# Optimization experiments

Measured on AMD Instinct MI355X. Metric: run time of the kernel, lower is better.

## Reference

```python
import jax, jax.numpy as jnp
import numpy as np

B, T, F, H, L = 256, 512, 64, 256, 2
DH = 2 * H          # decoder hidden size (bidirectional encoder concat)
OUT, OSL = 2, 20    # output_size, output_seq_len


def gru_cell(x, h, Wih, Whh, bih, bhh):
    # PyTorch GRU cell, gate order (r, z, n)
    gi = x @ Wih.T + bih
    gh = h @ Whh.T + bhh
    ir, iz, inn = jnp.split(gi, 3, axis=-1)
    hr, hz, hn = jnp.split(gh, 3, axis=-1)
    r = jax.nn.sigmoid(ir + hr)
    z = jax.nn.sigmoid(iz + hz)
    n = jnp.tanh(inn + r * hn)
    return (1.0 - z) * n + z * h


def setup_inputs() -> dict:
    key = jax.random.key(0)
    ks = iter(jax.random.split(key, 32))
    def p(shape, scale=0.05):
        return jax.random.normal(next(ks), shape, dtype=jnp.float32) * scale
    inp = {
        "x": p((B, T, F), 1.0),
        "start_token": jnp.zeros((1, 1, OUT), jnp.float32),
        # encoder layer 0 (input F), layer 1 (input 2H); axis 0 = direction (fwd, bwd)
        "enc_Wih0": p((2, 3 * H, F)), "enc_Whh0": p((2, 3 * H, H)),
        "enc_bih0": p((2, 3 * H)),   "enc_bhh0": p((2, 3 * H)),
        "enc_Wih1": p((2, 3 * H, 2 * H)), "enc_Whh1": p((2, 3 * H, H)),
        "enc_bih1": p((2, 3 * H)),   "enc_bhh1": p((2, 3 * H)),
        # decoder: unidirectional, hidden DH; layer0 input OUT, layer1 input DH
        "dec_Wih0": p((3 * DH, OUT)), "dec_Whh0": p((3 * DH, DH)),
        "dec_bih0": p((3 * DH,)),    "dec_bhh0": p((3 * DH,)),
        "dec_Wih1": p((3 * DH, DH)), "dec_Whh1": p((3 * DH, DH)),
        "dec_bih1": p((3 * DH,)),    "dec_bhh1": p((3 * DH,)),
        "fc_W": p((OUT, DH)), "fc_b": p((OUT,)),
    }
    return inp


def _run_dir(xs, Wih, Whh, bih, bhh, reverse):
    # xs: [T, B, Fin] -> (ys [T, B, H], h_T [B, H])
    h0 = jnp.zeros((xs.shape[1], Whh.shape[1]), xs.dtype)
    def step(h, xt):
        hn = gru_cell(xt, h, Wih, Whh, bih, bhh)
        return hn, hn
    hT, ys = jax.lax.scan(step, h0, xs, reverse=reverse)
    return ys, hT


def reference(x, start_token,
              enc_Wih0, enc_Whh0, enc_bih0, enc_bhh0,
              enc_Wih1, enc_Whh1, enc_bih1, enc_bhh1,
              dec_Wih0, dec_Whh0, dec_bih0, dec_bhh0,
              dec_Wih1, dec_Whh1, dec_bih1, dec_bhh1,
              fc_W, fc_b):
    b = x.shape[0]
    xs = jnp.swapaxes(x, 0, 1)  # [T, B, F]
    enc_layers = [(enc_Wih0, enc_Whh0, enc_bih0, enc_bhh0),
                  (enc_Wih1, enc_Whh1, enc_bih1, enc_bhh1)]
    hiddens = []
    layer_in = xs
    for (Wih, Whh, bih, bhh) in enc_layers:
        yf, hf = _run_dir(layer_in, Wih[0], Whh[0], bih[0], bhh[0], reverse=False)
        yb, hb = _run_dir(layer_in, Wih[1], Whh[1], bih[1], bhh[1], reverse=True)
        layer_in = jnp.concatenate([yf, yb], axis=-1)   # [T, B, 2H]
        hiddens.append(jnp.concatenate([hf, hb], axis=-1))  # [B, 2H] = cat(fwd, bwd)
    inp0 = jnp.broadcast_to(start_token, (b, 1, OUT))[:, 0]  # [B, OUT]
    def dec_step(carry, _):
        inp, (h0, h1) = carry
        h0n = gru_cell(inp, h0, dec_Wih0, dec_Whh0, dec_bih0, dec_bhh0)
        h1n = gru_cell(h0n, h1, dec_Wih1, dec_Whh1, dec_bih1, dec_bhh1)
        pred = h1n @ fc_W.T + fc_b
        return (pred, (h0n, h1n)), pred
    _, preds = jax.lax.scan(dec_step, (inp0, (hiddens[0], hiddens[1])), None, length=OSL)
    return jnp.swapaxes(preds, 0, 1)  # [B, OSL, OUT]
```

## Files before the change

### kernel.cpp

```cpp
#include <hip/hip_runtime.h>
#include <hip/hip_bf16.h>
#include <stdint.h>
#include <stddef.h>


typedef __bf16 bf16_t;
typedef bf16_t bf16x8 __attribute__((ext_vector_type(8)));
typedef float  f32x4  __attribute__((ext_vector_type(4)));

#define B_   256
#define T_   512
#define F_   64
#define H_   256
#define G_   768
#define DH_  512
#define DG_  1536
#define OSL_ 20

__device__ __forceinline__ float sigm(float x) {
    float e = __builtin_amdgcn_exp2f(-1.442695040888963f * x);
    return __builtin_amdgcn_rcpf(1.0f + e);
}
__device__ __forceinline__ float tanh_(float x) {
    float e = __builtin_amdgcn_exp2f(-2.885390081777927f * x);
    return __builtin_amdgcn_rcpf(1.0f + e) * 2.0f - 1.0f;
}

__device__ __forceinline__ bf16x8 load_f32x8_as_bf16(const float* p) {
    f32x4 u = *(const f32x4*)p;
    f32x4 v = *(const f32x4*)(p + 4);
    bf16x8 r;
    r[0]=(bf16_t)u[0]; r[1]=(bf16_t)u[1]; r[2]=(bf16_t)u[2]; r[3]=(bf16_t)u[3];
    r[4]=(bf16_t)v[0]; r[5]=(bf16_t)v[1]; r[6]=(bf16_t)v[2]; r[7]=(bf16_t)v[3];
    return r;
}


__global__ void cast_f32_bf16(const float* __restrict__ src, bf16_t* __restrict__ dst, int n) {
    int i = blockIdx.x * 256 + threadIdx.x;
    if (i < n) dst[i] = (bf16_t)src[i];
}

__global__ void weff_prep(const float* __restrict__ wih0d, const float* __restrict__ fcw,
                          const float* __restrict__ fcb, const float* __restrict__ bih0d,
                          const float* __restrict__ st, bf16_t* __restrict__ weff,
                          float* __restrict__ beff, float* __restrict__ ov) {
    int tid = blockIdx.x * 256 + threadIdx.x;
    if (tid >= DG_ * DH_) return;
    int g = tid >> 9, k = tid & 511;
    float a0 = wih0d[g * 2], a1 = wih0d[g * 2 + 1];
    weff[tid] = (bf16_t)(a0 * fcw[k] + a1 * fcw[DH_ + k]);
    if (k == 0) {
        beff[g] = a0 * fcb[0] + a1 * fcb[1] + bih0d[g];
        ov[g]   = a0 * st[0]  + a1 * st[1]  + bih0d[g];
    }
}

__global__ __launch_bounds__(256) void gemm_gi(
    const float* __restrict__ x, const bf16_t* __restrict__ xcat,
    const bf16_t* __restrict__ Bt, bf16_t* __restrict__ gi, int t0, int K) {
    __shared__ bf16_t As[128 * 64];
    __shared__ bf16_t Bs[128 * 64];
    int m0 = blockIdx.x * 128, n0 = blockIdx.y * 128;
    int tid = threadIdx.x;
    int lane = tid & 63, w = tid >> 6;
    int col = lane & 15, quad = lane >> 4;
    int qm = (w >> 1) * 64, qn = (w & 1) * 64;

    int tl = m0 >> 8;
    int bbase = m0 & 255;
    int t_real = t0 + tl;
    if (n0 >= 768) t_real = (T_ - 1) - t_real;

    f32x4 acc[4][4] = {};
    for (int k0 = 0; k0 < K; k0 += 64) {
        __syncthreads();
#pragma unroll
        for (int i = 0; i < 4; i++) {
            int c = i * 256 + tid;
            int m = c >> 3, kc = c & 7;
            int kcs = kc ^ (m & 7);
            bf16x8 av;
            if (K == 64) {
                av = load_f32x8_as_bf16(x + ((size_t)(bbase + m) * T_ + t_real) * F_ + kcs * 8);
            } else {
                av = *(const bf16x8*)(xcat + ((size_t)t_real * B_ + bbase + m) * DH_ + k0 + kcs * 8);
            }
            *(bf16x8*)(&As[c * 8]) = av;
            *(bf16x8*)(&Bs[c * 8]) = *(const bf16x8*)(Bt + (size_t)(n0 + m) * K + k0 + kcs * 8);
        }
        __syncthreads();
#pragma unroll
        for (int kt = 0; kt < 2; kt++) {
            bf16x8 a[4], b[4];
#pragma unroll
            for (int mt = 0; mt < 4; mt++) {
                int r = qm + mt * 16 + col;
                a[mt] = *(const bf16x8*)(&As[(r * 8 + ((kt * 4 + quad) ^ (r & 7))) * 8]);
                int rn = qn + mt * 16 + col;
                b[mt] = *(const bf16x8*)(&Bs[(rn * 8 + ((kt * 4 + quad) ^ (rn & 7))) * 8]);
            }
#pragma unroll
            for (int mt = 0; mt < 4; mt++)
#pragma unroll
                for (int nt = 0; nt < 4; nt++)
                    acc[mt][nt] = __builtin_amdgcn_mfma_f32_16x16x32_bf16(a[mt], b[nt], acc[mt][nt], 0, 0, 0);
        }
    }
#pragma unroll
    for (int mt = 0; mt < 4; mt++)
#pragma unroll
        for (int nt = 0; nt < 4; nt++)
#pragma unroll
            for (int i = 0; i < 4; i++) {
                int row = m0 + qm + mt * 16 + quad * 4 + i;
                int cg  = n0 + qn + nt * 16 + col;
                gi[(size_t)row * DG_ + cg] = (bf16_t)acc[mt][nt][i];
            }
}

__global__ __launch_bounds__(512) void gru_scan(
    const bf16_t* __restrict__ gi, int t0, int tc,
    const bf16_t* __restrict__ whh,
    const float* __restrict__ bih, const float* __restrict__ bhh,
    float* __restrict__ hstate, bf16_t* __restrict__ y, float* __restrict__ hT) {
    __shared__ bf16_t gi_lds[16 * 768];
    __shared__ bf16_t h_lds[2 * 16 * 264];

    int dir = blockIdx.x >> 4;
    int b0  = (blockIdx.x & 15) * 16;
    int tid = threadIdx.x;
    int w = tid >> 6, lane = tid & 63, col = lane & 15, quad = lane >> 4;

    bf16x8 wf[3][2][8];
    const bf16_t* wbase = whh + (size_t)dir * G_ * H_;
#pragma unroll
    for (int g = 0; g < 3; g++)
#pragma unroll
        for (int nt = 0; nt < 2; nt++) {
            int row = g * 256 + w * 32 + nt * 16 + col;
#pragma unroll
            for (int kt = 0; kt < 8; kt++)
                wf[g][nt][kt] = *(const bf16x8*)(wbase + (size_t)row * H_ + kt * 32 + quad * 8);
        }
    float brz[2][2], bin_[2], bhn[2];
#pragma unroll
    for (int nt = 0; nt < 2; nt++) {
        int j = w * 32 + nt * 16 + col;
        brz[0][nt] = bih[dir * G_ + j] + bhh[dir * G_ + j];
        brz[1][nt] = bih[dir * G_ + 256 + j] + bhh[dir * G_ + 256 + j];
        bin_[nt]   = bih[dir * G_ + 512 + j];
        bhn[nt]    = bhh[dir * G_ + 512 + j];
    }
    int bb[3], oo[3];
#pragma unroll
    for (int it = 0; it < 3; it++) {
        int c = it * 512 + tid;
        bb[it] = c / 96;
        oo[it] = (c % 96) * 8;
    }
    float hold[2][4];
#pragma unroll
    for (int nt = 0; nt < 2; nt++)
#pragma unroll
        for (int i = 0; i < 4; i++) {
            int j = w * 32 + nt * 16 + col;
            hold[nt][i] = t0 ? hstate[dir * 65536 + (b0 + quad * 4 + i) * 256 + j] : 0.0f;
        }
    for (int i = tid; i < 16 * 264; i += 512) {
        int b = i / 264, j = i % 264;
        float v = (t0 && j < 256) ? hstate[dir * 65536 + (b0 + b) * 256 + j] : 0.0f;
        h_lds[i] = (bf16_t)v;
    }
#pragma unroll
    for (int it = 0; it < 3; it++) {
        int c = it * 512 + tid;
        *(bf16x8*)(&gi_lds[c * 8]) =
            *(const bf16x8*)(gi + ((size_t)0 * B_ + b0 + bb[it]) * DG_ + dir * G_ + oo[it]);
    }
    __syncthreads();

    for (int s = 0; s < tc; s++) {
        int par = s & 1;
        int t = t0 + s;
        int sn = (s + 1 < tc) ? (s + 1) : s;

        bf16x8 pg[3];
#pragma unroll
        for (int it = 0; it < 3; it++)
            pg[it] = *(const bf16x8*)(gi + ((size_t)sn * B_ + b0 + bb[it]) * DG_ + dir * G_ + oo[it]);

        f32x4 acc[3][2] = {};
        const bf16_t* hcur = &h_lds[par * 4224];
#pragma unroll
        for (int kt = 0; kt < 8; kt++) {
            bf16x8 af = *(const bf16x8*)(hcur + col * 264 + kt * 32 + quad * 8);
#pragma unroll
            for (int g = 0; g < 3; g++)
#pragma unroll
                for (int nt = 0; nt < 2; nt++)
                    acc[g][nt] = __builtin_amdgcn_mfma_f32_16x16x32_bf16(af, wf[g][nt][kt], acc[g][nt], 0, 0, 0);
        }

        bf16_t* hnext = &h_lds[(par ^ 1) * 4224];
        int tp = dir ? (T_ - 1 - t) : t;
#pragma unroll
        for (int nt = 0; nt < 2; nt++) {
            int j = w * 32 + nt * 16 + col;
#pragma unroll
            for (int i = 0; i < 4; i++) {
                int b = quad * 4 + i;
                float gr = acc[0][nt][i] + (float)gi_lds[b * 768 + j]       + brz[0][nt];
                float gz = acc[1][nt][i] + (float)gi_lds[b * 768 + 256 + j] + brz[1][nt];
                float gn = (float)gi_lds[b * 768 + 512 + j] + bin_[nt];
                float r = sigm(gr), z = sigm(gz);
                float n = tanh_(gn + r * (acc[2][nt][i] + bhn[nt]));
                float hv = (1.0f - z) * n + z * hold[nt][i];
                hold[nt][i] = hv;
                hnext[b * 264 + j] = (bf16_t)hv;
                if (y) y[((size_t)tp * B_ + b0 + b) * DH_ + dir * H_ + j] = (bf16_t)hv;
                if (t == T_ - 1) hT[(size_t)(b0 + b) * DH_ + dir * H_ + j] = hv;
            }
        }
        __syncthreads();
#pragma unroll
        for (int it = 0; it < 3; it++)
            *(bf16x8*)(&gi_lds[(it * 512 + tid) * 8]) = pg[it];
        __syncthreads();
    }
#pragma unroll
    for (int nt = 0; nt < 2; nt++)
#pragma unroll
        for (int i = 0; i < 4; i++) {
            int j = w * 32 + nt * 16 + col;
            hstate[dir * 65536 + (b0 + quad * 4 + i) * 256 + j] = hold[nt][i];
        }
}

__global__ __launch_bounds__(256) void dec_cell(
    const float* __restrict__ xsrc, const bf16_t* __restrict__ Wx,
    const float* __restrict__ bx, const float* __restrict__ ov,
    const float* __restrict__ hin, const bf16_t* __restrict__ Wh,
    const float* __restrict__ bh, float* __restrict__ hout,
    float* __restrict__ hist) {
    int jblk = blockIdx.x & 7;
    int b0   = (blockIdx.x >> 3) * 16;
    int tid = threadIdx.x, w = tid >> 6, lane = tid & 63, col = lane & 15, quad = lane >> 4;
    int j = jblk * 64 + w * 16 + col;
    bool do_gi = (ov == nullptr);

    f32x4 agi[3] = {}, agh[3] = {};
#pragma unroll 4
    for (int kt = 0; kt < 16; kt++) {
        bf16x8 ah = load_f32x8_as_bf16(hin + (size_t)(b0 + col) * DH_ + kt * 32 + quad * 8);
#pragma unroll
        for (int g = 0; g < 3; g++) {
            bf16x8 bw = *(const bf16x8*)(Wh + (size_t)(g * DH_ + j) * DH_ + kt * 32 + quad * 8);
            agh[g] = __builtin_amdgcn_mfma_f32_16x16x32_bf16(ah, bw, agh[g], 0, 0, 0);
        }
        if (do_gi) {
            bf16x8 ax = load_f32x8_as_bf16(xsrc + (size_t)(b0 + col) * DH_ + kt * 32 + quad * 8);
#pragma unroll
            for (int g = 0; g < 3; g++) {
                bf16x8 bw = *(const bf16x8*)(Wx + (size_t)(g * DH_ + j) * DH_ + kt * 32 + quad * 8);
                agi[g] = __builtin_amdgcn_mfma_f32_16x16x32_bf16(ax, bw, agi[g], 0, 0, 0);
            }
        }
    }
#pragma unroll
    for (int i = 0; i < 4; i++) {
        int b = b0 + quad * 4 + i;
        float gr, gz, gn;
        if (do_gi) {
            gr = agi[0][i] + bx[j];
            gz = agi[1][i] + bx[DH_ + j];
            gn = agi[2][i] + bx[2 * DH_ + j];
        } else {
            gr = ov[j]; gz = ov[DH_ + j]; gn = ov[2 * DH_ + j];
        }
        float hr = agh[0][i] + bh[j];
        float hz = agh[1][i] + bh[DH_ + j];
        float hn = agh[2][i] + bh[2 * DH_ + j];
        float r = sigm(gr + hr), z = sigm(gz + hz);
        float n = tanh_(gn + r * hn);
        float hold = hin[(size_t)b * DH_ + j];
        float hv = (1.0f - z) * n + z * hold;
        hout[(size_t)b * DH_ + j] = hv;
        if (hist) hist[(size_t)b * DH_ + j] = hv;
    }
}

__global__ __launch_bounds__(256) void fc_all(
    const float* __restrict__ hist, const float* __restrict__ fcw,
    const float* __restrict__ fcb, float* __restrict__ out) {
    int t  = blockIdx.x >> 4;
    int b0 = (blockIdx.x & 15) * 16;
    int tid = threadIdx.x;
    int bl = tid >> 4, o = (tid >> 3) & 1, part = tid & 7;
    const float* hp = hist + ((size_t)t * B_ + b0 + bl) * DH_;
    const float* wp = fcw + o * DH_;
    float s = 0.0f;
    for (int k = part * 64; k < part * 64 + 64; k += 4) {
        f32x4 hv = *(const f32x4*)(hp + k);
        f32x4 wv = *(const f32x4*)(wp + k);
        s += hv[0] * wv[0] + hv[1] * wv[1] + hv[2] * wv[2] + hv[3] * wv[3];
    }
    s += __shfl_down(s, 4); s += __shfl_down(s, 2); s += __shfl_down(s, 1);
    if (part == 0) out[(size_t)(b0 + bl) * (OSL_ * 2) + t * 2 + o] = s + fcb[o];
}


#define OFF_WIH0E 0ull
#define OFF_WHH0E 196608ull
#define OFF_WIH1E 983040ull
#define OFF_WHH1E 2555904ull
#define OFF_WDHH0 3342336ull
#define OFF_WDIH1 4915200ull
#define OFF_WDHH1 6488064ull
#define OFF_WEFF  8060928ull
#define OFF_BEFF  9633792ull
#define OFF_OV    9658368ull
#define OFF_H0A   9682944ull
#define OFF_H0B   10207232ull
#define OFF_H1A   10731520ull
#define OFF_H1B   11255808ull
#define OFF_HST   11780096ull
#define OFF_HIST  12304384ull
#define OFF_XCAT  22790144ull
#define OFF_GI    157007872ull

extern "C" void kernel_launch(void* const* d_in, const int* in_sizes, int n_in,
                              void* d_out, int out_size, void* d_ws, size_t ws_size,
                              hipStream_t stream) {
    const float* x      = (const float*)d_in[0];
    const float* st     = (const float*)d_in[1];
    const float* eWih0  = (const float*)d_in[2];
    const float* eWhh0  = (const float*)d_in[3];
    const float* ebih0  = (const float*)d_in[4];
    const float* ebhh0  = (const float*)d_in[5];
    const float* eWih1  = (const float*)d_in[6];
    const float* eWhh1  = (const float*)d_in[7];
    const float* ebih1  = (const float*)d_in[8];
    const float* ebhh1  = (const float*)d_in[9];
    const float* dWih0  = (const float*)d_in[10];
    const float* dWhh0  = (const float*)d_in[11];
    const float* dbih0  = (const float*)d_in[12];
    const float* dbhh0  = (const float*)d_in[13];
    const float* dWih1  = (const float*)d_in[14];
    const float* dWhh1  = (const float*)d_in[15];
    const float* dbih1  = (const float*)d_in[16];
    const float* dbhh1  = (const float*)d_in[17];
    const float* fcW    = (const float*)d_in[18];
    const float* fcb    = (const float*)d_in[19];

    char* ws = (char*)d_ws;
    bf16_t* wih0e = (bf16_t*)(ws + OFF_WIH0E);
    bf16_t* whh0e = (bf16_t*)(ws + OFF_WHH0E);
    bf16_t* wih1e = (bf16_t*)(ws + OFF_WIH1E);
    bf16_t* whh1e = (bf16_t*)(ws + OFF_WHH1E);
    bf16_t* wdhh0 = (bf16_t*)(ws + OFF_WDHH0);
    bf16_t* wdih1 = (bf16_t*)(ws + OFF_WDIH1);
    bf16_t* wdhh1 = (bf16_t*)(ws + OFF_WDHH1);
    bf16_t* weff  = (bf16_t*)(ws + OFF_WEFF);
    float*  beff  = (float*)(ws + OFF_BEFF);
    float*  ovp   = (float*)(ws + OFF_OV);
    float*  h0buf[2] = { (float*)(ws + OFF_H0A), (float*)(ws + OFF_H0B) };
    float*  h1buf[2] = { (float*)(ws + OFF_H1A), (float*)(ws + OFF_H1B) };
    float*  hstate = (float*)(ws + OFF_HST);
    float*  hist  = (float*)(ws + OFF_HIST);
    bf16_t* xcat  = (bf16_t*)(ws + OFF_XCAT);
    bf16_t* gi    = (bf16_t*)(ws + OFF_GI);

    int Tc = 512;
    while (Tc > 8 && OFF_GI + (unsigned long long)Tc * 786432ull > (unsigned long long)ws_size)
        Tc >>= 1;
    int nch = T_ / Tc;

    cast_f32_bf16<<<(2*G_*F_ + 255)/256, 256, 0, stream>>>(eWih0, wih0e, 2*G_*F_);
    cast_f32_bf16<<<(2*G_*H_ + 255)/256, 256, 0, stream>>>(eWhh0, whh0e, 2*G_*H_);
    cast_f32_bf16<<<(2*G_*DH_ + 255)/256, 256, 0, stream>>>(eWih1, wih1e, 2*G_*DH_);
    cast_f32_bf16<<<(2*G_*H_ + 255)/256, 256, 0, stream>>>(eWhh1, whh1e, 2*G_*H_);
    cast_f32_bf16<<<(DG_*DH_ + 255)/256, 256, 0, stream>>>(dWhh0, wdhh0, DG_*DH_);
    cast_f32_bf16<<<(DG_*DH_ + 255)/256, 256, 0, stream>>>(dWih1, wdih1, DG_*DH_);
    cast_f32_bf16<<<(DG_*DH_ + 255)/256, 256, 0, stream>>>(dWhh1, wdhh1, DG_*DH_);
    weff_prep<<<(DG_*DH_ + 255)/256, 256, 0, stream>>>(dWih0, fcW, fcb, dbih0, st, weff, beff, ovp);

    for (int c = 0; c < nch; c++) {
        gemm_gi<<<dim3(Tc * 2, 12), 256, 0, stream>>>(x, nullptr, wih0e, gi, c * Tc, 64);
        gru_scan<<<32, 512, 0, stream>>>(gi, c * Tc, Tc, whh0e, ebih0, ebhh0, hstate, xcat, h0buf[0]);
    }
    for (int c = 0; c < nch; c++) {
        gemm_gi<<<dim3(Tc * 2, 12), 256, 0, stream>>>(nullptr, xcat, wih1e, gi, c * Tc, 512);
        gru_scan<<<32, 512, 0, stream>>>(gi, c * Tc, Tc, whh1e, ebih1, ebhh1, hstate, nullptr, h1buf[0]);
    }

    int p0 = 0, p1 = 0;
    for (int t = 0; t < OSL_; t++) {
        dec_cell<<<128, 256, 0, stream>>>(h1buf[p1], weff, beff, (t == 0 ? ovp : nullptr),
                                          h0buf[p0], wdhh0, dbhh0, h0buf[p0 ^ 1], nullptr);
        p0 ^= 1;
        dec_cell<<<128, 256, 0, stream>>>(h0buf[p0], wdih1, dbih1, nullptr,
                                          h1buf[p1], wdhh1, dbhh1, h1buf[p1 ^ 1],
                                          hist + (size_t)t * B_ * DH_);
        p1 ^= 1;
    }
    fc_all<<<OSL_ * 16, 256, 0, stream>>>(hist, fcW, fcb, (float*)d_out);
}
```

Measured before the change: 4.916 ms.

## Async global-to-LDS copies and single-barrier GRU scan step with deferred y stores

The projection GEMM and the GRU scan now stage operands with global_load_lds async copies instead of going through registers. The scan double-buffers the input-gate tile in LDS and keeps one h buffer. Each step loads h into registers before a single barrier, which removes the second __syncthreads per timestep. The y output is written as vectorised 16-byte stores of the previous step's h taken from LDS, and the GRU blend is rewritten as n + z*(h-n). The risk is correctness: the hand-written wait only covers lgkmcnt, so it is unclear the async vmcnt-tracked copies complete before the data is read.

```diff
diff --git a/kernel.cpp b/kernel.cpp
--- a/kernel.cpp
+++ b/kernel.cpp
@@ -33,6 +33,12 @@
     r[0]=(bf16_t)u[0]; r[1]=(bf16_t)u[1]; r[2]=(bf16_t)u[2]; r[3]=(bf16_t)u[3];
     r[4]=(bf16_t)v[0]; r[5]=(bf16_t)v[1]; r[6]=(bf16_t)v[2]; r[7]=(bf16_t)v[3];
     return r;
+}
+
+__device__ __forceinline__ void async_cp16(const bf16_t* g, bf16_t* l) {
+    __builtin_amdgcn_global_load_lds(
+        (const __attribute__((address_space(1))) unsigned int*)g,
+        (__attribute__((address_space(3))) unsigned int*)l, 16, 0, 0);
 }
 
 
@@ -80,14 +86,14 @@
             int c = i * 256 + tid;
             int m = c >> 3, kc = c & 7;
             int kcs = kc ^ (m & 7);
-            bf16x8 av;
             if (K == 64) {
-                av = load_f32x8_as_bf16(x + ((size_t)(bbase + m) * T_ + t_real) * F_ + kcs * 8);
+                *(bf16x8*)(&As[c * 8]) =
+                    load_f32x8_as_bf16(x + ((size_t)(bbase + m) * T_ + t_real) * F_ + kcs * 8);
             } else {
-                av = *(const bf16x8*)(xcat + ((size_t)t_real * B_ + bbase + m) * DH_ + k0 + kcs * 8);
+                async_cp16(xcat + ((size_t)t_real * B_ + bbase + m) * DH_ + k0 + kcs * 8,
+                           &As[c * 8]);
             }
-            *(bf16x8*)(&As[c * 8]) = av;
-            *(bf16x8*)(&Bs[c * 8]) = *(const bf16x8*)(Bt + (size_t)(n0 + m) * K + k0 + kcs * 8);
+            async_cp16(Bt + (size_t)(n0 + m) * K + k0 + kcs * 8, &Bs[c * 8]);
         }
         __syncthreads();
 #pragma unroll
@@ -124,8 +130,8 @@
     const bf16_t* __restrict__ whh,
     const float* __restrict__ bih, const float* __restrict__ bhh,
     float* __restrict__ hstate, bf16_t* __restrict__ y, float* __restrict__ hT) {
-    __shared__ bf16_t gi_lds[16 * 768];
-    __shared__ bf16_t h_lds[2 * 16 * 264];
+    __shared__ bf16_t gi_lds[2 * 16 * 768];
+    __shared__ bf16_t h_lds[16 * 264];
 
     int dir = blockIdx.x >> 4;
     int b0  = (blockIdx.x & 15) * 16;
@@ -175,58 +181,70 @@
 #pragma unroll
     for (int it = 0; it < 3; it++) {
         int c = it * 512 + tid;
-        *(bf16x8*)(&gi_lds[c * 8]) =
-            *(const bf16x8*)(gi + ((size_t)0 * B_ + b0 + bb[it]) * DG_ + dir * G_ + oo[it]);
+        async_cp16(gi + ((size_t)0 * B_ + b0 + bb[it]) * DG_ + dir * G_ + oo[it],
+                   &gi_lds[c * 8]);
     }
     __syncthreads();
 
     for (int s = 0; s < tc; s++) {
         int par = s & 1;
         int t = t0 + s;
+
+        if (y && s > 0) {
+            int tprev = dir ? (T_ - t) : (t - 1);
+            int b = tid >> 5, off = (tid & 31) * 8;
+            bf16x8 hv = *(const bf16x8*)(&h_lds[b * 264 + off]);
+            *(bf16x8*)(y + ((size_t)tprev * B_ + b0 + b) * DH_ + dir * H_ + off) = hv;
+        }
+
         int sn = (s + 1 < tc) ? (s + 1) : s;
-
-        bf16x8 pg[3];
 #pragma unroll
         for (int it = 0; it < 3; it++)
-            pg[it] = *(const bf16x8*)(gi + ((size_t)sn * B_ + b0 + bb[it]) * DG_ + dir * G_ + oo[it]);
+            async_cp16(gi + ((size_t)sn * B_ + b0 + bb[it]) * DG_ + dir * G_ + oo[it],
+                       &gi_lds[(par ^ 1) * 12288 + ((it * 512 + tid) * 8)]);
+
+        bf16x8 af[8];
+#pragma unroll
+        for (int kt = 0; kt < 8; kt++)
+            af[kt] = *(const bf16x8*)(&h_lds[col * 264 + kt * 32 + quad * 8]);
+
+        asm volatile("s_waitcnt lgkmcnt(0)\n\ts_barrier" ::: "memory");
 
         f32x4 acc[3][2] = {};
-        const bf16_t* hcur = &h_lds[par * 4224];
-#pragma unroll
-        for (int kt = 0; kt < 8; kt++) {
-            bf16x8 af = *(const bf16x8*)(hcur + col * 264 + kt * 32 + quad * 8);
+#pragma unroll
+        for (int kt = 0; kt < 8; kt++)
 #pragma unroll
             for (int g = 0; g < 3; g++)
 #pragma unroll
                 for (int nt = 0; nt < 2; nt++)
-                    acc[g][nt] = __builtin_amdgcn_mfma_f32_16x16x32_bf16(af, wf[g][nt][kt], acc[g][nt], 0, 0, 0);
-        }
-
-        bf16_t* hnext = &h_lds[(par ^ 1) * 4224];
-        int tp = dir ? (T_ - 1 - t) : t;
+                    acc[g][nt] = __builtin_amdgcn_mfma_f32_16x16x32_bf16(af[kt], wf[g][nt][kt], acc[g][nt], 0, 0, 0);
+
+        const bf16_t* gcur = &gi_lds[par * 12288];
 #pragma unroll
         for (int nt = 0; nt < 2; nt++) {
             int j = w * 32 + nt * 16 + col;
 #pragma unroll
             for (int i = 0; i < 4; i++) {
                 int b = quad * 4 + i;
-                float gr = acc[0][nt][i] + (float)gi_lds[b * 768 + j]       + brz[0][nt];
-                float gz = acc[1][nt][i] + (float)gi_lds[b * 768 + 256 + j] + brz[1][nt];
-                float gn = (float)gi_lds[b * 768 + 512 + j] + bin_[nt];
+                float gr = acc[0][nt][i] + (float)gcur[b * 768 + j]       + brz[0][nt];
+                float gz = acc[1][nt][i] + (float)gcur[b * 768 + 256 + j] + brz[1][nt];
+                float gn = (float)gcur[b * 768 + 512 + j] + bin_[nt];
                 float r = sigm(gr), z = sigm(gz);
                 float n = tanh_(gn + r * (acc[2][nt][i] + bhn[nt]));
-                float hv = (1.0f - z) * n + z * hold[nt][i];
+                float hv = n + z * (hold[nt][i] - n);
                 hold[nt][i] = hv;
-                hnext[b * 264 + j] = (bf16_t)hv;
-                if (y) y[((size_t)tp * B_ + b0 + b) * DH_ + dir * H_ + j] = (bf16_t)hv;
+                h_lds[b * 264 + j] = (bf16_t)hv;
                 if (t == T_ - 1) hT[(size_t)(b0 + b) * DH_ + dir * H_ + j] = hv;
             }
         }
         __syncthreads();
-#pragma unroll
-        for (int it = 0; it < 3; it++)
-            *(bf16x8*)(&gi_lds[(it * 512 + tid) * 8]) = pg[it];
-        __syncthreads();
+    }
+    if (y) {
+        int tlast = t0 + tc - 1;
+        int tp = dir ? (T_ - 1 - tlast) : tlast;
+        int b = tid >> 5, off = (tid & 31) * 8;
+        bf16x8 hv = *(const bf16x8*)(&h_lds[b * 264 + off]);
+        *(bf16x8*)(y + ((size_t)tp * B_ + b0 + b) * DH_ + dir * H_ + off) = hv;
     }
 #pragma unroll
     for (int nt = 0; nt < 2; nt++)
@@ -284,7 +302,7 @@
         float r = sigm(gr + hr), z = sigm(gz + hz);
         float n = tanh_(gn + r * hn);
         float hold = hin[(size_t)b * DH_ + j];
-        float hv = (1.0f - z) * n + z * hold;
+        float hv = n + z * (hold - n);
         hout[(size_t)b * DH_ + j] = hv;
         if (hist) hist[(size_t)b * DH_ + j] = hv;
     }
```

Result: slower. 5.246 ms (+6.7%).
